# Kernel optimization log

Hardware: AMD Instinct MI355X
Metric: run time of the kernel (lower is better)

Reference implementation:

```python
import jax, jax.numpy as jnp
import numpy as np


def setup_inputs() -> dict:
    key = jax.random.key(0)
    k0, k1, k2, k3, k4 = jax.random.split(key, 5)
    B, d_inner, L, d_state = 64, 384, 197, 16
    x = jax.random.normal(k0, (B, d_inner, L), dtype=jnp.float32)
    # deltaA = exp(delta*A) lies in (0,1); uniform keeps the recurrence stable
    deltaA = jax.random.uniform(k1, (B, d_inner, L, d_state), dtype=jnp.float32)
    deltaB = jax.random.normal(k2, (B, d_inner, L, d_state), dtype=jnp.float32)
    C = jax.random.normal(k3, (B, d_state, L), dtype=jnp.float32)
    D = jax.random.normal(k4, (d_inner,), dtype=jnp.float32)
    return {"x": x, "deltaA": deltaA, "deltaB": deltaB, "C": C, "D": D}


def reference(x, deltaA, deltaB, C, D):
    """Selective scan: h_t = deltaB_t*x_t + deltaA_t*h_{t-1}; y_t = h_t @ C_t.
    x:(B,d,L) deltaA/deltaB:(B,d,L,n) C:(B,n,L) D:(d,)
    """
    deltaB_x = deltaB * x[..., None]              # (B,d,L,n)
    dA_t = jnp.moveaxis(deltaA, 2, 0)             # (L,B,d,n)
    dBx_t = jnp.moveaxis(deltaB_x, 2, 0)          # (L,B,d,n)
    C_t = jnp.moveaxis(C, 2, 0)                   # (L,B,n)

    def step(h, inputs):
        a, bx, c = inputs
        h = bx + a * h                            # (B,d,n)
        y = jnp.einsum("bdn,bn->bd", h, c)        # (B,d)
        return h, y

    h0 = jnp.zeros(dA_t.shape[1:], dtype=x.dtype)
    _, ys = jax.lax.scan(step, h0, (dA_t, dBx_t, C_t))  # ys: (L,B,d)
    y = jnp.moveaxis(ys, 0, 2)                    # (B,d,L)
    return y + x * D[:, None]
```

## Files before the change

### kernel.cpp

```cpp
#include <hip/hip_runtime.h>


#define B_   64
#define DIN  384
#define L_   197
#define N_   16
#define CSTR 20
#define NCH  12

template<int CTRL>
__device__ __forceinline__ float dppmov(float src, float oldv) {
    return __int_as_float(__builtin_amdgcn_update_dpp(
        __float_as_int(oldv), __float_as_int(src), CTRL, 0xF, 0xF, false));
}
__device__ __forceinline__ float qsum(float p) {
    p += __int_as_float(__builtin_amdgcn_update_dpp(0, __float_as_int(p), 0xB1, 0xF, 0xF, true));
    p += __int_as_float(__builtin_amdgcn_update_dpp(0, __float_as_int(p), 0x4E, 0xF, 0xF, true));
    return p;
}
__device__ __forceinline__ float bcast12q(float v) {
    return __int_as_float(__builtin_amdgcn_ds_swizzle(__float_as_int(v), 0x193));
}

__global__ __launch_bounds__(256, 2)
void ssm_pscan(const float* __restrict__ x, const float* __restrict__ dA,
               const float* __restrict__ dB, const float* __restrict__ C,
               const float* __restrict__ D, float* __restrict__ y)
{
    __shared__ __align__(16) float Cs[L_ * CSTR];

    const int tid = threadIdx.x;
    const int b   = blockIdx.y;

    const float* Cg = C + (size_t)b * (N_ * L_);
    for (int i = tid; i < N_ * L_; i += 256) {
        const int n = i / L_;
        const int t = i - n * L_;
        Cs[t * CSTR + n] = Cg[i];
    }
    __syncthreads();

    const int lane = tid & 63;
    const int wav  = tid >> 6;
    const int row  = lane >> 4;
    const int p    = lane & 15;
    const int p4   = p >> 2;
    const int q    = p & 3;

    const int d   = blockIdx.x * 16 + wav * 4 + row;
    const size_t bd = (size_t)b * DIN + d;

    const float* Arow = dA + bd * (size_t)(L_ * N_);
    const float* Brow = dB + bd * (size_t)(L_ * N_);
    const float* Xrow = x  + bd * L_;
    float*       Yrow = y  + bd * L_;
    const float  Dd   = D[d];
    const int laneAB  = p4 * 64 + q * 4;
    const float* CsQ  = Cs + q * 4;

    float hcx = 0.f, hcy = 0.f, hcz = 0.f, hcw = 0.f;

    float4 PA0,PA1,PA2,PA3, PB0,PB1,PB2,PB3;
    float4 QA0,QA1,QA2,QA3, QB0,QB1,QB2,QB3;
    float  Px0,Px1,Px2,Px3, Qx0,Qx1,Qx2,Qx3;

#define LOADC(Pfx, c) do { \
    const float* _a = Arow + (c)*256 + laneAB; \
    const float* _g = Brow + (c)*256 + laneAB; \
    Pfx##A0 = *(const float4*)(_a +  0); Pfx##A1 = *(const float4*)(_a + 16); \
    Pfx##A2 = *(const float4*)(_a + 32); Pfx##A3 = *(const float4*)(_a + 48); \
    Pfx##B0 = *(const float4*)(_g +  0); Pfx##B1 = *(const float4*)(_g + 16); \
    Pfx##B2 = *(const float4*)(_g + 32); Pfx##B3 = *(const float4*)(_g + 48); \
    const float* _x = Xrow + (c)*16 + p4*4; \
    Pfx##x0 = _x[0]; Pfx##x1 = _x[1]; Pfx##x2 = _x[2]; Pfx##x3 = _x[3]; \
} while (0)

#define LOADT(Pfx) do { \
    const int _tb = 192 + p4*4; \
    const int _t0 = _tb   > 196 ? 196 : _tb; \
    const int _t1 = _tb+1 > 196 ? 196 : _tb+1; \
    const int _t2 = _tb+2 > 196 ? 196 : _tb+2; \
    const int _t3 = _tb+3 > 196 ? 196 : _tb+3; \
    Pfx##A0 = *(const float4*)(Arow + _t0*16 + q*4); \
    Pfx##A1 = *(const float4*)(Arow + _t1*16 + q*4); \
    Pfx##A2 = *(const float4*)(Arow + _t2*16 + q*4); \
    Pfx##A3 = *(const float4*)(Arow + _t3*16 + q*4); \
    Pfx##B0 = *(const float4*)(Brow + _t0*16 + q*4); \
    Pfx##B1 = *(const float4*)(Brow + _t1*16 + q*4); \
    Pfx##B2 = *(const float4*)(Brow + _t2*16 + q*4); \
    Pfx##B3 = *(const float4*)(Brow + _t3*16 + q*4); \
    Pfx##x0 = Xrow[_t0]; Pfx##x1 = Xrow[_t1]; \
    Pfx##x2 = Xrow[_t2]; Pfx##x3 = Xrow[_t3]; \
} while (0)

#define SCANE(Pfx, E) do { \
    Pfx##B0.E *= Pfx##x0; Pfx##B1.E *= Pfx##x1; \
    Pfx##B2.E *= Pfx##x2; Pfx##B3.E *= Pfx##x3; \
    Pfx##B1.E = fmaf(Pfx##A1.E, Pfx##B0.E, Pfx##B1.E); Pfx##A1.E *= Pfx##A0.E; \
    Pfx##B2.E = fmaf(Pfx##A2.E, Pfx##B1.E, Pfx##B2.E); Pfx##A2.E *= Pfx##A1.E; \
    Pfx##B3.E = fmaf(Pfx##A3.E, Pfx##B2.E, Pfx##B3.E); Pfx##A3.E *= Pfx##A2.E; \
    float _ta = Pfx##A3.E, _tv = Pfx##B3.E; \
    { float _pa = dppmov<0x114>(_ta, 1.0f), _pb = dppmov<0x114>(_tv, 0.0f); \
      _tv = fmaf(_ta, _pb, _tv); _ta *= _pa; } \
    { float _pa = dppmov<0x118>(_ta, 1.0f), _pb = dppmov<0x118>(_tv, 0.0f); \
      _tv = fmaf(_ta, _pb, _tv); _ta *= _pa; } \
    const float _Ea = dppmov<0x114>(_ta, 1.0f); \
    const float _Eb = dppmov<0x114>(_tv, 0.0f); \
    const float _s  = fmaf(_Ea, hc##E, _Eb); \
    Pfx##B0.E = fmaf(Pfx##A0.E, _s, Pfx##B0.E); \
    Pfx##B1.E = fmaf(Pfx##A1.E, _s, Pfx##B1.E); \
    Pfx##B2.E = fmaf(Pfx##A2.E, _s, Pfx##B2.E); \
    Pfx##B3.E = fmaf(Pfx##A3.E, _s, Pfx##B3.E); \
} while (0)

#define YJ(Pfx, j, tcj, yf) do { \
    const float4 _c4 = *(const float4*)(CsQ + (tcj)*CSTR); \
    float _yp = fmaf(Pfx##B##j.x, _c4.x, fmaf(Pfx##B##j.y, _c4.y, \
                 fmaf(Pfx##B##j.z, _c4.z, Pfx##B##j.w * _c4.w))); \
    _yp = qsum(_yp); \
    yf = fmaf(Pfx##x##j, Dd, _yp); \
} while (0)

#define COMPUTE(Pfx, c, TAIL) do { \
    SCANE(Pfx, x); SCANE(Pfx, y); SCANE(Pfx, z); SCANE(Pfx, w); \
    const int _t0s = (TAIL) ? (192 + p4*4) : ((c)*16 + p4*4); \
    int _c0 = _t0s, _c1 = _t0s+1, _c2 = _t0s+2, _c3 = _t0s+3; \
    if (TAIL) { _c0 = _c0>196?196:_c0; _c1 = _c1>196?196:_c1; \
                _c2 = _c2>196?196:_c2; _c3 = _c3>196?196:_c3; } \
    float _yf0,_yf1,_yf2,_yf3; \
    YJ(Pfx, 0, _c0, _yf0); YJ(Pfx, 1, _c1, _yf1); \
    YJ(Pfx, 2, _c2, _yf2); YJ(Pfx, 3, _c3, _yf3); \
    hcx = bcast12q(Pfx##B3.x); hcy = bcast12q(Pfx##B3.y); \
    hcz = bcast12q(Pfx##B3.z); hcw = bcast12q(Pfx##B3.w); \
    const float _ys = (q==0) ? _yf0 : (q==1) ? _yf1 : (q==2) ? _yf2 : _yf3; \
    if (!(TAIL) || p4 == 0 || (p4 == 1 && q == 0)) Yrow[_t0s + q] = _ys; \
} while (0)

    LOADC(P, 0);
#pragma unroll 1
    for (int c = 0; c < NCH; c += 2) {
        LOADC(Q, c + 1);
        __builtin_amdgcn_sched_barrier(0);
        COMPUTE(P, c, 0);
        if (c + 2 < NCH) { LOADC(P, c + 2); } else { LOADT(P); }
        __builtin_amdgcn_sched_barrier(0);
        COMPUTE(Q, c + 1, 0);
    }
    COMPUTE(P, 0, 1);

#undef COMPUTE
#undef YJ
#undef SCANE
#undef LOADT
#undef LOADC
}

extern "C" void kernel_launch(void* const* d_in, const int* in_sizes, int n_in,
                              void* d_out, int out_size, void* d_ws, size_t ws_size,
                              hipStream_t stream) {
    const float* x  = (const float*)d_in[0];
    const float* dA = (const float*)d_in[1];
    const float* dB = (const float*)d_in[2];
    const float* C  = (const float*)d_in[3];
    const float* D  = (const float*)d_in[4];
    float* yo = (float*)d_out;

    dim3 grid(DIN / 16, B_);
    dim3 block(256);
    ssm_pscan<<<grid, block, 0, stream>>>(x, dA, dB, C, D, yo);
}
```

Baseline: 155.1 us.

## Drop software double-buffering in favor of higher occupancy via thread-level parallelism

Removes the explicit two-stage register prefetch (P/Q buffers with sched barriers) so each chunk is loaded then computed in sequence, and raises launch bounds from 2 to 6 blocks per CU. The intent is to cut register pressure so more waves are resident, hiding memory latency through TLP instead of ILP within a wave. The risk is that each wave now stalls on its loads, and LDS usage (about 15.8KB per block) or registers may still cap how many blocks actually fit.

```diff
diff --git a/kernel.cpp b/kernel.cpp
--- a/kernel.cpp
+++ b/kernel.cpp
@@ -22,10 +22,10 @@
     return __int_as_float(__builtin_amdgcn_ds_swizzle(__float_as_int(v), 0x193));
 }
 
-__global__ __launch_bounds__(256, 2)
-void ssm_pscan(const float* __restrict__ x, const float* __restrict__ dA,
-               const float* __restrict__ dB, const float* __restrict__ C,
-               const float* __restrict__ D, float* __restrict__ y)
+__global__ __launch_bounds__(256, 6)
+void ssm_tlp(const float* __restrict__ x, const float* __restrict__ dA,
+             const float* __restrict__ dB, const float* __restrict__ C,
+             const float* __restrict__ D, float* __restrict__ y)
 {
     __shared__ __align__(16) float Cs[L_ * CSTR];
 
@@ -60,46 +60,43 @@
 
     float hcx = 0.f, hcy = 0.f, hcz = 0.f, hcw = 0.f;
 
-    float4 PA0,PA1,PA2,PA3, PB0,PB1,PB2,PB3;
-    float4 QA0,QA1,QA2,QA3, QB0,QB1,QB2,QB3;
-    float  Px0,Px1,Px2,Px3, Qx0,Qx1,Qx2,Qx3;
+    float4 A0,A1,A2,A3, G0,G1,G2,G3;
+    float  x0,x1,x2,x3;
 
-#define LOADC(Pfx, c) do { \
+#define LOADC(c) do { \
     const float* _a = Arow + (c)*256 + laneAB; \
     const float* _g = Brow + (c)*256 + laneAB; \
-    Pfx##A0 = *(const float4*)(_a +  0); Pfx##A1 = *(const float4*)(_a + 16); \
-    Pfx##A2 = *(const float4*)(_a + 32); Pfx##A3 = *(const float4*)(_a + 48); \
-    Pfx##B0 = *(const float4*)(_g +  0); Pfx##B1 = *(const float4*)(_g + 16); \
-    Pfx##B2 = *(const float4*)(_g + 32); Pfx##B3 = *(const float4*)(_g + 48); \
+    A0 = *(const float4*)(_a +  0); A1 = *(const float4*)(_a + 16); \
+    A2 = *(const float4*)(_a + 32); A3 = *(const float4*)(_a + 48); \
+    G0 = *(const float4*)(_g +  0); G1 = *(const float4*)(_g + 16); \
+    G2 = *(const float4*)(_g + 32); G3 = *(const float4*)(_g + 48); \
     const float* _x = Xrow + (c)*16 + p4*4; \
-    Pfx##x0 = _x[0]; Pfx##x1 = _x[1]; Pfx##x2 = _x[2]; Pfx##x3 = _x[3]; \
+    x0 = _x[0]; x1 = _x[1]; x2 = _x[2]; x3 = _x[3]; \
 } while (0)
 
-#define LOADT(Pfx) do { \
+#define LOADT() do { \
     const int _tb = 192 + p4*4; \
     const int _t0 = _tb   > 196 ? 196 : _tb; \
     const int _t1 = _tb+1 > 196 ? 196 : _tb+1; \
     const int _t2 = _tb+2 > 196 ? 196 : _tb+2; \
     const int _t3 = _tb+3 > 196 ? 196 : _tb+3; \
-    Pfx##A0 = *(const float4*)(Arow + _t0*16 + q*4); \
-    Pfx##A1 = *(const float4*)(Arow + _t1*16 + q*4); \
-    Pfx##A2 = *(const float4*)(Arow + _t2*16 + q*4); \
-    Pfx##A3 = *(const float4*)(Arow + _t3*16 + q*4); \
-    Pfx##B0 = *(const float4*)(Brow + _t0*16 + q*4); \
-    Pfx##B1 = *(const float4*)(Brow + _t1*16 + q*4); \
-    Pfx##B2 = *(const float4*)(Brow + _t2*16 + q*4); \
-    Pfx##B3 = *(const float4*)(Brow + _t3*16 + q*4); \
-    Pfx##x0 = Xrow[_t0]; Pfx##x1 = Xrow[_t1]; \
-    Pfx##x2 = Xrow[_t2]; Pfx##x3 = Xrow[_t3]; \
+    A0 = *(const float4*)(Arow + _t0*16 + q*4); \
+    A1 = *(const float4*)(Arow + _t1*16 + q*4); \
+    A2 = *(const float4*)(Arow + _t2*16 + q*4); \
+    A3 = *(const float4*)(Arow + _t3*16 + q*4); \
+    G0 = *(const float4*)(Brow + _t0*16 + q*4); \
+    G1 = *(const float4*)(Brow + _t1*16 + q*4); \
+    G2 = *(const float4*)(Brow + _t2*16 + q*4); \
+    G3 = *(const float4*)(Brow + _t3*16 + q*4); \
+    x0 = Xrow[_t0]; x1 = Xrow[_t1]; x2 = Xrow[_t2]; x3 = Xrow[_t3]; \
 } while (0)
 
-#define SCANE(Pfx, E) do { \
-    Pfx##B0.E *= Pfx##x0; Pfx##B1.E *= Pfx##x1; \
-    Pfx##B2.E *= Pfx##x2; Pfx##B3.E *= Pfx##x3; \
-    Pfx##B1.E = fmaf(Pfx##A1.E, Pfx##B0.E, Pfx##B1.E); Pfx##A1.E *= Pfx##A0.E; \
-    Pfx##B2.E = fmaf(Pfx##A2.E, Pfx##B1.E, Pfx##B2.E); Pfx##A2.E *= Pfx##A1.E; \
-    Pfx##B3.E = fmaf(Pfx##A3.E, Pfx##B2.E, Pfx##B3.E); Pfx##A3.E *= Pfx##A2.E; \
-    float _ta = Pfx##A3.E, _tv = Pfx##B3.E; \
+#define SCANE(E) do { \
+    G0.E *= x0; G1.E *= x1; G2.E *= x2; G3.E *= x3; \
+    G1.E = fmaf(A1.E, G0.E, G1.E); A1.E *= A0.E; \
+    G2.E = fmaf(A2.E, G1.E, G2.E); A2.E *= A1.E; \
+    G3.E = fmaf(A3.E, G2.E, G3.E); A3.E *= A2.E; \
+    float _ta = A3.E, _tv = G3.E; \
     { float _pa = dppmov<0x114>(_ta, 1.0f), _pb = dppmov<0x114>(_tv, 0.0f); \
       _tv = fmaf(_ta, _pb, _tv); _ta *= _pa; } \
     { float _pa = dppmov<0x118>(_ta, 1.0f), _pb = dppmov<0x118>(_tv, 0.0f); \
@@ -107,46 +104,42 @@
     const float _Ea = dppmov<0x114>(_ta, 1.0f); \
     const float _Eb = dppmov<0x114>(_tv, 0.0f); \
     const float _s  = fmaf(_Ea, hc##E, _Eb); \
-    Pfx##B0.E = fmaf(Pfx##A0.E, _s, Pfx##B0.E); \
-    Pfx##B1.E = fmaf(Pfx##A1.E, _s, Pfx##B1.E); \
-    Pfx##B2.E = fmaf(Pfx##A2.E, _s, Pfx##B2.E); \
-    Pfx##B3.E = fmaf(Pfx##A3.E, _s, Pfx##B3.E); \
+    G0.E = fmaf(A0.E, _s, G0.E); \
+    G1.E = fmaf(A1.E, _s, G1.E); \
+    G2.E = fmaf(A2.E, _s, G2.E); \
+    G3.E = fmaf(A3.E, _s, G3.E); \
 } while (0)
 
-#define YJ(Pfx, j, tcj, yf) do { \
+#define YJ(j, tcj, yf) do { \
     const float4 _c4 = *(const float4*)(CsQ + (tcj)*CSTR); \
-    float _yp = fmaf(Pfx##B##j.x, _c4.x, fmaf(Pfx##B##j.y, _c4.y, \
-                 fmaf(Pfx##B##j.z, _c4.z, Pfx##B##j.w * _c4.w))); \
+    float _yp = fmaf(G##j.x, _c4.x, fmaf(G##j.y, _c4.y, \
+                 fmaf(G##j.z, _c4.z, G##j.w * _c4.w))); \
     _yp = qsum(_yp); \
-    yf = fmaf(Pfx##x##j, Dd, _yp); \
+    yf = fmaf(x##j, Dd, _yp); \
 } while (0)
 
-#define COMPUTE(Pfx, c, TAIL) do { \
-    SCANE(Pfx, x); SCANE(Pfx, y); SCANE(Pfx, z); SCANE(Pfx, w); \
+#define COMPUTE(c, TAIL) do { \
+    SCANE(x); SCANE(y); SCANE(z); SCANE(w); \
     const int _t0s = (TAIL) ? (192 + p4*4) : ((c)*16 + p4*4); \
     int _c0 = _t0s, _c1 = _t0s+1, _c2 = _t0s+2, _c3 = _t0s+3; \
     if (TAIL) { _c0 = _c0>196?196:_c0; _c1 = _c1>196?196:_c1; \
                 _c2 = _c2>196?196:_c2; _c3 = _c3>196?196:_c3; } \
     float _yf0,_yf1,_yf2,_yf3; \
-    YJ(Pfx, 0, _c0, _yf0); YJ(Pfx, 1, _c1, _yf1); \
-    YJ(Pfx, 2, _c2, _yf2); YJ(Pfx, 3, _c3, _yf3); \
-    hcx = bcast12q(Pfx##B3.x); hcy = bcast12q(Pfx##B3.y); \
-    hcz = bcast12q(Pfx##B3.z); hcw = bcast12q(Pfx##B3.w); \
+    YJ(0, _c0, _yf0); YJ(1, _c1, _yf1); \
+    YJ(2, _c2, _yf2); YJ(3, _c3, _yf3); \
+    hcx = bcast12q(G3.x); hcy = bcast12q(G3.y); \
+    hcz = bcast12q(G3.z); hcw = bcast12q(G3.w); \
     const float _ys = (q==0) ? _yf0 : (q==1) ? _yf1 : (q==2) ? _yf2 : _yf3; \
     if (!(TAIL) || p4 == 0 || (p4 == 1 && q == 0)) Yrow[_t0s + q] = _ys; \
 } while (0)
 
-    LOADC(P, 0);
 #pragma unroll 1
-    for (int c = 0; c < NCH; c += 2) {
-        LOADC(Q, c + 1);
-        __builtin_amdgcn_sched_barrier(0);
-        COMPUTE(P, c, 0);
-        if (c + 2 < NCH) { LOADC(P, c + 2); } else { LOADT(P); }
-        __builtin_amdgcn_sched_barrier(0);
-        COMPUTE(Q, c + 1, 0);
+    for (int c = 0; c < NCH; ++c) {
+        LOADC(c);
+        COMPUTE(c, 0);
     }
-    COMPUTE(P, 0, 1);
+    LOADT();
+    COMPUTE(0, 1);
 
 #undef COMPUTE
 #undef YJ
@@ -167,5 +160,5 @@
 
     dim3 grid(DIN / 16, B_);
     dim3 block(256);
-    ssm_pscan<<<grid, block, 0, stream>>>(x, dA, dB, C, D, yo);
+    ssm_tlp<<<grid, block, 0, stream>>>(x, dA, dB, C, D, yo);
 }
```

New measurement: 145.1 us. 1.07x faster.

## Issue dA/dB loads via inline asm, stage x in LDS, raise occupancy

Applied to the files above, without the earlier changes.

Replaces compiler-generated float4 loads of deltaA/deltaB with inline-asm global_load_dwordx4 plus explicit s_waitcnt vmcnt(0), so the double-buffered prefetch is controlled by hand. The x rows for the block are staged in shared memory once instead of being loaded per chunk. Launch bounds go from 2 to 4 waves per SIMD to allow more blocks in flight. Risks: the full vmcnt(0) waits block until all outstanding loads finish, LDS use grows (about 28KB per block), and the higher occupancy target may force register limits.

```diff
diff --git a/kernel.cpp b/kernel.cpp
--- a/kernel.cpp
+++ b/kernel.cpp
@@ -5,8 +5,11 @@
 #define DIN  384
 #define L_   197
 #define N_   16
+#define LN   (L_ * N_)
 #define CSTR 20
 #define NCH  12
+
+typedef float f4 __attribute__((ext_vector_type(4)));
 
 template<int CTRL>
 __device__ __forceinline__ float dppmov(float src, float oldv) {
@@ -22,22 +25,34 @@
     return __int_as_float(__builtin_amdgcn_ds_swizzle(__float_as_int(v), 0x193));
 }
 
-__global__ __launch_bounds__(256, 2)
-void ssm_pscan(const float* __restrict__ x, const float* __restrict__ dA,
-               const float* __restrict__ dB, const float* __restrict__ C,
-               const float* __restrict__ D, float* __restrict__ y)
+#define GL4(dst, base, OFF) \
+    asm volatile("global_load_dwordx4 %0, %1, off offset:" #OFF \
+                 : "=v"(dst) : "v"(base) : "memory")
+
+#define WAITVM0() do { \
+    asm volatile("s_waitcnt vmcnt(0)" ::: "memory"); \
+    __builtin_amdgcn_sched_barrier(0); \
+} while (0)
+
+__global__ __launch_bounds__(256, 4)
+void ssm_asml(const float* __restrict__ x, const float* __restrict__ dA,
+              const float* __restrict__ dB, const float* __restrict__ C,
+              const float* __restrict__ D, float* __restrict__ y)
 {
     __shared__ __align__(16) float Cs[L_ * CSTR];
+    __shared__ float Xs[16 * L_];
 
     const int tid = threadIdx.x;
     const int b   = blockIdx.y;
 
-    const float* Cg = C + (size_t)b * (N_ * L_);
-    for (int i = tid; i < N_ * L_; i += 256) {
+    const float* Cg = C + (size_t)b * LN;
+    for (int i = tid; i < LN; i += 256) {
         const int n = i / L_;
         const int t = i - n * L_;
         Cs[t * CSTR + n] = Cg[i];
     }
+    const float* Xg = x + ((size_t)b * DIN + blockIdx.x * 16) * L_;
+    for (int i = tid; i < 16 * L_; i += 256) Xs[i] = Xg[i];
     __syncthreads();
 
     const int lane = tid & 63;
@@ -50,29 +65,26 @@
     const int d   = blockIdx.x * 16 + wav * 4 + row;
     const size_t bd = (size_t)b * DIN + d;
 
-    const float* Arow = dA + bd * (size_t)(L_ * N_);
-    const float* Brow = dB + bd * (size_t)(L_ * N_);
-    const float* Xrow = x  + bd * L_;
+    const float* Arow = dA + bd * (size_t)LN;
+    const float* Brow = dB + bd * (size_t)LN;
     float*       Yrow = y  + bd * L_;
     const float  Dd   = D[d];
     const int laneAB  = p4 * 64 + q * 4;
     const float* CsQ  = Cs + q * 4;
+    const float* XsL  = Xs + (wav * 4 + row) * L_ + p4 * 4;
 
     float hcx = 0.f, hcy = 0.f, hcz = 0.f, hcw = 0.f;
 
-    float4 PA0,PA1,PA2,PA3, PB0,PB1,PB2,PB3;
-    float4 QA0,QA1,QA2,QA3, QB0,QB1,QB2,QB3;
-    float  Px0,Px1,Px2,Px3, Qx0,Qx1,Qx2,Qx3;
+    f4 PA0,PA1,PA2,PA3, PG0,PG1,PG2,PG3;
+    f4 QA0,QA1,QA2,QA3, QG0,QG1,QG2,QG3;
 
 #define LOADC(Pfx, c) do { \
     const float* _a = Arow + (c)*256 + laneAB; \
     const float* _g = Brow + (c)*256 + laneAB; \
-    Pfx##A0 = *(const float4*)(_a +  0); Pfx##A1 = *(const float4*)(_a + 16); \
-    Pfx##A2 = *(const float4*)(_a + 32); Pfx##A3 = *(const float4*)(_a + 48); \
-    Pfx##B0 = *(const float4*)(_g +  0); Pfx##B1 = *(const float4*)(_g + 16); \
-    Pfx##B2 = *(const float4*)(_g + 32); Pfx##B3 = *(const float4*)(_g + 48); \
-    const float* _x = Xrow + (c)*16 + p4*4; \
-    Pfx##x0 = _x[0]; Pfx##x1 = _x[1]; Pfx##x2 = _x[2]; Pfx##x3 = _x[3]; \
+    GL4(Pfx##A0, _a, 0);   GL4(Pfx##A1, _a, 64); \
+    GL4(Pfx##A2, _a, 128); GL4(Pfx##A3, _a, 192); \
+    GL4(Pfx##G0, _g, 0);   GL4(Pfx##G1, _g, 64); \
+    GL4(Pfx##G2, _g, 128); GL4(Pfx##G3, _g, 192); \
 } while (0)
 
 #define LOADT(Pfx) do { \
@@ -81,25 +93,22 @@
     const int _t1 = _tb+1 > 196 ? 196 : _tb+1; \
     const int _t2 = _tb+2 > 196 ? 196 : _tb+2; \
     const int _t3 = _tb+3 > 196 ? 196 : _tb+3; \
-    Pfx##A0 = *(const float4*)(Arow + _t0*16 + q*4); \
-    Pfx##A1 = *(const float4*)(Arow + _t1*16 + q*4); \
-    Pfx##A2 = *(const float4*)(Arow + _t2*16 + q*4); \
-    Pfx##A3 = *(const float4*)(Arow + _t3*16 + q*4); \
-    Pfx##B0 = *(const float4*)(Brow + _t0*16 + q*4); \
-    Pfx##B1 = *(const float4*)(Brow + _t1*16 + q*4); \
-    Pfx##B2 = *(const float4*)(Brow + _t2*16 + q*4); \
-    Pfx##B3 = *(const float4*)(Brow + _t3*16 + q*4); \
-    Pfx##x0 = Xrow[_t0]; Pfx##x1 = Xrow[_t1]; \
-    Pfx##x2 = Xrow[_t2]; Pfx##x3 = Xrow[_t3]; \
+    GL4(Pfx##A0, Arow + _t0*16 + q*4, 0); \
+    GL4(Pfx##A1, Arow + _t1*16 + q*4, 0); \
+    GL4(Pfx##A2, Arow + _t2*16 + q*4, 0); \
+    GL4(Pfx##A3, Arow + _t3*16 + q*4, 0); \
+    GL4(Pfx##G0, Brow + _t0*16 + q*4, 0); \
+    GL4(Pfx##G1, Brow + _t1*16 + q*4, 0); \
+    GL4(Pfx##G2, Brow + _t2*16 + q*4, 0); \
+    GL4(Pfx##G3, Brow + _t3*16 + q*4, 0); \
 } while (0)
 
 #define SCANE(Pfx, E) do { \
-    Pfx##B0.E *= Pfx##x0; Pfx##B1.E *= Pfx##x1; \
-    Pfx##B2.E *= Pfx##x2; Pfx##B3.E *= Pfx##x3; \
-    Pfx##B1.E = fmaf(Pfx##A1.E, Pfx##B0.E, Pfx##B1.E); Pfx##A1.E *= Pfx##A0.E; \
-    Pfx##B2.E = fmaf(Pfx##A2.E, Pfx##B1.E, Pfx##B2.E); Pfx##A2.E *= Pfx##A1.E; \
-    Pfx##B3.E = fmaf(Pfx##A3.E, Pfx##B2.E, Pfx##B3.E); Pfx##A3.E *= Pfx##A2.E; \
-    float _ta = Pfx##A3.E, _tv = Pfx##B3.E; \
+    Pfx##G0.E *= x0; Pfx##G1.E *= x1; Pfx##G2.E *= x2; Pfx##G3.E *= x3; \
+    Pfx##G1.E = fmaf(Pfx##A1.E, Pfx##G0.E, Pfx##G1.E); Pfx##A1.E *= Pfx##A0.E; \
+    Pfx##G2.E = fmaf(Pfx##A2.E, Pfx##G1.E, Pfx##G2.E); Pfx##A2.E *= Pfx##A1.E; \
+    Pfx##G3.E = fmaf(Pfx##A3.E, Pfx##G2.E, Pfx##G3.E); Pfx##A3.E *= Pfx##A2.E; \
+    float _ta = Pfx##A3.E, _tv = Pfx##G3.E; \
     { float _pa = dppmov<0x114>(_ta, 1.0f), _pb = dppmov<0x114>(_tv, 0.0f); \
       _tv = fmaf(_ta, _pb, _tv); _ta *= _pa; } \
     { float _pa = dppmov<0x118>(_ta, 1.0f), _pb = dppmov<0x118>(_tv, 0.0f); \
@@ -107,44 +116,50 @@
     const float _Ea = dppmov<0x114>(_ta, 1.0f); \
     const float _Eb = dppmov<0x114>(_tv, 0.0f); \
     const float _s  = fmaf(_Ea, hc##E, _Eb); \
-    Pfx##B0.E = fmaf(Pfx##A0.E, _s, Pfx##B0.E); \
-    Pfx##B1.E = fmaf(Pfx##A1.E, _s, Pfx##B1.E); \
-    Pfx##B2.E = fmaf(Pfx##A2.E, _s, Pfx##B2.E); \
-    Pfx##B3.E = fmaf(Pfx##A3.E, _s, Pfx##B3.E); \
+    Pfx##G0.E = fmaf(Pfx##A0.E, _s, Pfx##G0.E); \
+    Pfx##G1.E = fmaf(Pfx##A1.E, _s, Pfx##G1.E); \
+    Pfx##G2.E = fmaf(Pfx##A2.E, _s, Pfx##G2.E); \
+    Pfx##G3.E = fmaf(Pfx##A3.E, _s, Pfx##G3.E); \
 } while (0)
 
-#define YJ(Pfx, j, tcj, yf) do { \
-    const float4 _c4 = *(const float4*)(CsQ + (tcj)*CSTR); \
-    float _yp = fmaf(Pfx##B##j.x, _c4.x, fmaf(Pfx##B##j.y, _c4.y, \
-                 fmaf(Pfx##B##j.z, _c4.z, Pfx##B##j.w * _c4.w))); \
+#define YJ(Pfx, j, tcj, xv, yf) do { \
+    const f4 _c4 = *(const f4*)(CsQ + (tcj)*CSTR); \
+    float _yp = fmaf(Pfx##G##j.x, _c4.x, fmaf(Pfx##G##j.y, _c4.y, \
+                 fmaf(Pfx##G##j.z, _c4.z, Pfx##G##j.w * _c4.w))); \
     _yp = qsum(_yp); \
-    yf = fmaf(Pfx##x##j, Dd, _yp); \
+    yf = fmaf(xv, Dd, _yp); \
 } while (0)
 
 #define COMPUTE(Pfx, c, TAIL) do { \
-    SCANE(Pfx, x); SCANE(Pfx, y); SCANE(Pfx, z); SCANE(Pfx, w); \
     const int _t0s = (TAIL) ? (192 + p4*4) : ((c)*16 + p4*4); \
     int _c0 = _t0s, _c1 = _t0s+1, _c2 = _t0s+2, _c3 = _t0s+3; \
     if (TAIL) { _c0 = _c0>196?196:_c0; _c1 = _c1>196?196:_c1; \
                 _c2 = _c2>196?196:_c2; _c3 = _c3>196?196:_c3; } \
+    const float x0 = (TAIL) ? Xs[(wav*4+row)*L_ + _c0] : XsL[(c)*16 + 0]; \
+    const float x1 = (TAIL) ? Xs[(wav*4+row)*L_ + _c1] : XsL[(c)*16 + 1]; \
+    const float x2 = (TAIL) ? Xs[(wav*4+row)*L_ + _c2] : XsL[(c)*16 + 2]; \
+    const float x3 = (TAIL) ? Xs[(wav*4+row)*L_ + _c3] : XsL[(c)*16 + 3]; \
+    SCANE(Pfx, x); SCANE(Pfx, y); SCANE(Pfx, z); SCANE(Pfx, w); \
     float _yf0,_yf1,_yf2,_yf3; \
-    YJ(Pfx, 0, _c0, _yf0); YJ(Pfx, 1, _c1, _yf1); \
-    YJ(Pfx, 2, _c2, _yf2); YJ(Pfx, 3, _c3, _yf3); \
-    hcx = bcast12q(Pfx##B3.x); hcy = bcast12q(Pfx##B3.y); \
-    hcz = bcast12q(Pfx##B3.z); hcw = bcast12q(Pfx##B3.w); \
+    YJ(Pfx, 0, _c0, x0, _yf0); YJ(Pfx, 1, _c1, x1, _yf1); \
+    YJ(Pfx, 2, _c2, x2, _yf2); YJ(Pfx, 3, _c3, x3, _yf3); \
+    hcx = bcast12q(Pfx##G3.x); hcy = bcast12q(Pfx##G3.y); \
+    hcz = bcast12q(Pfx##G3.z); hcw = bcast12q(Pfx##G3.w); \
     const float _ys = (q==0) ? _yf0 : (q==1) ? _yf1 : (q==2) ? _yf2 : _yf3; \
     if (!(TAIL) || p4 == 0 || (p4 == 1 && q == 0)) Yrow[_t0s + q] = _ys; \
 } while (0)
 
     LOADC(P, 0);
+    WAITVM0();
+
 #pragma unroll 1
     for (int c = 0; c < NCH; c += 2) {
         LOADC(Q, c + 1);
-        __builtin_amdgcn_sched_barrier(0);
         COMPUTE(P, c, 0);
+        WAITVM0();
         if (c + 2 < NCH) { LOADC(P, c + 2); } else { LOADT(P); }
-        __builtin_amdgcn_sched_barrier(0);
         COMPUTE(Q, c + 1, 0);
+        WAITVM0();
     }
     COMPUTE(P, 0, 1);
 
@@ -167,5 +182,5 @@
 
     dim3 grid(DIN / 16, B_);
     dim3 block(256);
-    ssm_pscan<<<grid, block, 0, stream>>>(x, dA, dB, C, D, yo);
+    ssm_asml<<<grid, block, 0, stream>>>(x, dA, dB, C, D, yo);
 }
```

New measurement: 146.7 us. -5.4%, faster.
